# Performance work log

Hardware: AMD Instinct MI355X
Metric: run time of the kernel (lower is better)

The kernel has to match this reference:

```python
import jax, jax.numpy as jnp
import numpy as np

N_NODES = 150000
N_EDGES = 3000000
EMBED_DIM = 64
N_LAYERS = 3


def setup_inputs() -> dict:
    key = jax.random.key(0)
    k1, k2, k3, k4 = jax.random.split(key, 4)
    emb = jax.random.normal(k1, (N_NODES, EMBED_DIM), dtype=jnp.float32)
    sqrt_degree = jax.random.uniform(k2, (N_NODES, 1), dtype=jnp.float32)
    src = jax.random.randint(k3, (N_EDGES,), 0, N_NODES, dtype=jnp.int32)
    dst = jax.random.randint(k4, (N_EDGES,), 0, N_NODES, dtype=jnp.int32)
    return {"emb": emb, "sqrt_degree": sqrt_degree, "src": src, "dst": dst}


def _aggregate_unweighted(x, sqrt_degree, src, dst):
    # node = x * sqrt_degree ; message = node[src] ; N_h = sum per dst ; N_h *= sqrt_degree
    scaled = x * sqrt_degree                      # [N, D]
    msgs = scaled[src]                            # [E, D] gather
    agg = jax.ops.segment_sum(msgs, dst, num_segments=N_NODES)  # [N, D] scatter-add
    return agg * sqrt_degree


def reference(emb, sqrt_degree, src, dst):
    # propagate_embedding: ego embedding + n_layers of symmetric-normalized SpMM,
    # mean-combined across layers (layers_weight is None -> plain mean).
    ego = emb
    all_embed = [ego]
    for _ in range(N_LAYERS):
        ego = _aggregate_unweighted(ego, sqrt_degree, src, dst)
        all_embed.append(ego)
    return jnp.mean(jnp.stack(all_embed, axis=-1), axis=-1)  # [N, D]
```

## Files before the change

kernel.cpp:

```cpp
#include <hip/hip_runtime.h>

#define N_NODES   150000
#define N_EDGES   3000000
#define EMBED_DIM 64
#define N_UNITS   (N_EDGES / 4)
#define NREG      2344
#define CHUNK_U   2048
#define CHUNK_E   (CHUNK_U * 4)
#define NCB       ((N_UNITS + CHUNK_U - 1) / CHUNK_U)
#define REC_MAX   2560
#define KGRP      8
#define KPER      ((NCB + KGRP - 1) / KGRP)

typedef unsigned int uint;

__device__ inline uint pack2_bf16(float a, float b) {
    uint ua = __float_as_uint(a);
    uint ub = __float_as_uint(b);
    ua += 0x7fffu + ((ua >> 16) & 1u);
    ub += 0x7fffu + ((ub >> 16) & 1u);
    return (ua >> 16) | (ub & 0xffff0000u);
}
__device__ inline float bflo(uint u) { return __uint_as_float(u << 16); }
__device__ inline float bfhi(uint u) { return __uint_as_float(u & 0xffff0000u); }
#define FMA2(u, A0, A1)                                        \
    {   (A0) += w * bflo(u);  (A1) += w * bfhi(u); }

__global__ void k_to_y(const float4* __restrict__ in, const float* __restrict__ sd,
                       uint2* __restrict__ out, int n4) {
    int i = blockIdx.x * blockDim.x + threadIdx.x;
    if (i < n4) {
        float s = sd[i >> 4];
        float4 v = in[i];
        out[i] = make_uint2(pack2_bf16(s * v.x, s * v.y), pack2_bf16(s * v.z, s * v.w));
    }
}

__global__ __launch_bounds__(256) void k_count_place(const int4* __restrict__ dst4,
                                                     const int4* __restrict__ src4,
                                                     uint* __restrict__ bh,
                                                     uint* __restrict__ rowtot,
                                                     uint* __restrict__ bkt) {
    __shared__ uint cnt[NREG];
    __shared__ uint part[256];
    int t = threadIdx.x;
    for (int b = t; b < NREG; b += 256) cnt[b] = 0;
    __syncthreads();
    int base = blockIdx.x * CHUNK_U;
    for (int i = t; i < CHUNK_U; i += 256) {
        int u = base + i;
        if (u < N_UNITS) {
            int4 d = dst4[u];
            atomicAdd(&cnt[d.x >> 6], 1u);
            atomicAdd(&cnt[d.y >> 6], 1u);
            atomicAdd(&cnt[d.z >> 6], 1u);
            atomicAdd(&cnt[d.w >> 6], 1u);
        }
    }
    __syncthreads();
    const int CPT = (NREG + 255) / 256;
    int b0 = t * CPT, b1 = b0 + CPT; if (b1 > NREG) b1 = NREG; if (b0 > NREG) b0 = NREG;
    uint own = 0;
    for (int b = b0; b < b1; ++b) own += cnt[b];
    part[t] = own;
    __syncthreads();
    for (int off = 1; off < 256; off <<= 1) {
        uint v = (t >= off) ? part[t - off] : 0;
        __syncthreads();
        part[t] += v;
        __syncthreads();
    }
    uint run = part[t] - own;
    for (int b = b0; b < b1; ++b) { uint c = cnt[b]; cnt[b] = run; run += c; }
    __syncthreads();
    for (int b = t; b < NREG; b += 256) bh[blockIdx.x * NREG + b] = cnt[b];
    if (t == 255) rowtot[blockIdx.x] = part[255];
    __syncthreads();
    uint kbase = (uint)blockIdx.x * CHUNK_E;
    for (int i = t; i < CHUNK_U; i += 256) {
        int u = base + i;
        if (u < N_UNITS) {
            int4 d = dst4[u];
            int4 s = src4[u];
            uint p0 = atomicAdd(&cnt[d.x >> 6], 1u);
            uint p1 = atomicAdd(&cnt[d.y >> 6], 1u);
            uint p2 = atomicAdd(&cnt[d.z >> 6], 1u);
            uint p3 = atomicAdd(&cnt[d.w >> 6], 1u);
            bkt[kbase + p0] = ((uint)s.x << 6) | ((uint)d.x & 63u);
            bkt[kbase + p1] = ((uint)s.y << 6) | ((uint)d.y & 63u);
            bkt[kbase + p2] = ((uint)s.z << 6) | ((uint)d.z & 63u);
            bkt[kbase + p3] = ((uint)s.w << 6) | ((uint)d.w & 63u);
        }
    }
}

__global__ void k_cols(const uint* __restrict__ bh, const uint* __restrict__ rowtot,
                       uint* __restrict__ partial) {
    int tid = blockIdx.x * blockDim.x + threadIdx.x;
    if (tid >= KGRP * NREG) return;
    int g = tid / NREG;
    int r = tid % NREG;
    int kend = (g + 1) * KPER; if (kend > NCB) kend = NCB;
    uint run = 0;
    if (r + 1 < NREG) {
        for (int k = g * KPER; k < kend; ++k)
            run += bh[k * NREG + r + 1] - bh[k * NREG + r];
    } else {
        for (int k = g * KPER; k < kend; ++k)
            run += rowtot[k] - bh[k * NREG + r];
    }
    partial[g * NREG + r] = run;
}

__global__ void k_scan_small(const uint* __restrict__ partial, int* __restrict__ binPtr) {
    __shared__ uint s[1024];
    int t = threadIdx.x;
    int base = t * 3;
    uint v0 = 0, v1 = 0, v2 = 0;
    #pragma unroll
    for (int g = 0; g < KGRP; ++g) {
        if (base + 0 < NREG) v0 += partial[g * NREG + base + 0];
        if (base + 1 < NREG) v1 += partial[g * NREG + base + 1];
        if (base + 2 < NREG) v2 += partial[g * NREG + base + 2];
    }
    uint s3 = v0 + v1 + v2;
    s[t] = s3;
    __syncthreads();
    for (int off = 1; off < 1024; off <<= 1) {
        uint add = (t >= off) ? s[t - off] : 0;
        __syncthreads();
        s[t] += add;
        __syncthreads();
    }
    uint excl = s[t] - s3;
    if (base + 0 < NREG) binPtr[base + 0] = (int)excl;
    if (base + 1 < NREG) binPtr[base + 1] = (int)(excl + v0);
    if (base + 2 < NREG) binPtr[base + 2] = (int)(excl + v0 + v1);
    if (t == 1023) binPtr[NREG] = (int)s[1023];
}

__global__ __launch_bounds__(256) void k_finalize(const uint* __restrict__ bkt,
                                                  const uint* __restrict__ bh,
                                                  const uint* __restrict__ rowtot,
                                                  const int* __restrict__ binPtr,
                                                  int* __restrict__ rowptr,
                                                  uint* __restrict__ srcn) {
    __shared__ uint recs[REC_MAX];
    __shared__ uint part[256];
    __shared__ uint cnt64[64];
    __shared__ uint off64[64];
    int r = blockIdx.x;
    int t = threadIdx.x;
    int rbase = binPtr[r];
    int rcnt  = binPtr[r + 1] - rbase;

    int k0 = 2 * t, k1 = 2 * t + 1;
    uint s0 = 0, c0 = 0, s1 = 0, c1 = 0;
    if (k0 < NCB) {
        s0 = bh[k0 * NREG + r];
        uint e0 = (r + 1 < NREG) ? bh[k0 * NREG + r + 1] : rowtot[k0];
        c0 = e0 - s0;
    }
    if (k1 < NCB) {
        s1 = bh[k1 * NREG + r];
        uint e1 = (r + 1 < NREG) ? bh[k1 * NREG + r + 1] : rowtot[k1];
        c1 = e1 - s1;
    }
    uint own = c0 + c1;
    part[t] = own;
    __syncthreads();
    for (int off = 1; off < 256; off <<= 1) {
        uint v = (t >= off) ? part[t - off] : 0;
        __syncthreads();
        part[t] += v;
        __syncthreads();
    }
    uint w0 = part[t] - own;
    uint w1 = w0 + c0;
    for (uint i = 0; i < c0; ++i) recs[w0 + i] = bkt[(uint)k0 * CHUNK_E + s0 + i];
    for (uint i = 0; i < c1; ++i) recs[w1 + i] = bkt[(uint)k1 * CHUNK_E + s1 + i];
    if (t < 64) cnt64[t] = 0;
    __syncthreads();

    for (int e = t; e < rcnt; e += 256) atomicAdd(&cnt64[recs[e] & 63u], 1u);
    __syncthreads();
    if (t == 0) {
        uint run = 0;
        for (int i = 0; i < 64; ++i) { off64[i] = run; run += cnt64[i]; }
    }
    __syncthreads();
    int nbase = r * 64;
    int nloc = N_NODES - nbase; if (nloc > 64) nloc = 64;
    if (t < nloc) rowptr[nbase + t] = rbase + (int)off64[t];
    if (t < 64) cnt64[t] = 0;
    __syncthreads();

    for (int e = t; e < rcnt; e += 256) {
        uint rec = recs[e];
        uint loc = rec & 63u;
        uint pos = (uint)rbase + off64[loc] + atomicAdd(&cnt64[loc], 1u);
        srcn[pos] = rec >> 6;
    }
}

__global__ __launch_bounds__(256) void k_layer(const uint4* __restrict__ yb,
                                               const int* __restrict__ rowptr,
                                               const uint* __restrict__ srcn,
                                               const float* __restrict__ sd,
                                               uint4* __restrict__ yout) {
    int wv = (blockIdx.x * blockDim.x + threadIdx.x) >> 6;
    wv = __builtin_amdgcn_readfirstlane(wv);
    int nA = wv * 2;
    if (nA >= N_NODES) return;
    int nB = nA + 1;
    int lane = threadIdx.x & 63;
    int ep = lane >> 3;
    int j  = lane & 7;
    uint joff = (uint)j << 4;

    int startA = rowptr[nA];
    int endA   = rowptr[nB];
    int startB = endA;
    int endB   = (nB + 1 < N_NODES) ? rowptr[nB + 1] : N_EDGES;
    int eAm1 = max(endA - 1, 0);
    int eBm1 = max(endB - 1, 0);

    float a0 = 0.f, a1 = 0.f, a2 = 0.f, a3 = 0.f;
    float a4 = 0.f, a5 = 0.f, a6 = 0.f, a7 = 0.f;
    float b0 = 0.f, b1 = 0.f, b2 = 0.f, b3 = 0.f;
    float b4 = 0.f, b5 = 0.f, b6 = 0.f, b7 = 0.f;
    #pragma unroll 2
    for (int bA = startA, bB = startB; bA < endA || bB < endB; bA += 8, bB += 8) {
        int eeA = bA + ep;
        int eeB = bB + ep;
        int ecA = min(eeA, eAm1);
        int ecB = min(eeB, eBm1);
        uint sA = srcn[ecA];
        uint sB = srcn[ecB];
        float wA = (eeA < endA) ? 1.0f : 0.0f;
        float wB = (eeB < endB) ? 1.0f : 0.0f;
        uint4 vA = *(const uint4*)((const char*)yb + ((sA << 7) + joff));
        uint4 vB = *(const uint4*)((const char*)yb + ((sB << 7) + joff));
        { float w = wA;
          FMA2(vA.x, a0, a1); FMA2(vA.y, a2, a3); FMA2(vA.z, a4, a5); FMA2(vA.w, a6, a7); }
        { float w = wB;
          FMA2(vB.x, b0, b1); FMA2(vB.y, b2, b3); FMA2(vB.z, b4, b5); FMA2(vB.w, b6, b7); }
    }
    #pragma unroll
    for (int m = 8; m <= 32; m <<= 1) {
        a0 += __shfl_xor(a0, m, 64); a1 += __shfl_xor(a1, m, 64);
        a2 += __shfl_xor(a2, m, 64); a3 += __shfl_xor(a3, m, 64);
        a4 += __shfl_xor(a4, m, 64); a5 += __shfl_xor(a5, m, 64);
        a6 += __shfl_xor(a6, m, 64); a7 += __shfl_xor(a7, m, 64);
        b0 += __shfl_xor(b0, m, 64); b1 += __shfl_xor(b1, m, 64);
        b2 += __shfl_xor(b2, m, 64); b3 += __shfl_xor(b3, m, 64);
        b4 += __shfl_xor(b4, m, 64); b5 += __shfl_xor(b5, m, 64);
        b6 += __shfl_xor(b6, m, 64); b7 += __shfl_xor(b7, m, 64);
    }
    if (ep == 0) {
        float sdv = sd[nA];
        float s2 = sdv * sdv;
        uint4 r;
        r.x = pack2_bf16(s2 * a0, s2 * a1);
        r.y = pack2_bf16(s2 * a2, s2 * a3);
        r.z = pack2_bf16(s2 * a4, s2 * a5);
        r.w = pack2_bf16(s2 * a6, s2 * a7);
        yout[(size_t)nA * 8 + j] = r;
    } else if (ep == 1) {
        float sdv = sd[nB];
        float s2 = sdv * sdv;
        uint4 r;
        r.x = pack2_bf16(s2 * b0, s2 * b1);
        r.y = pack2_bf16(s2 * b2, s2 * b3);
        r.z = pack2_bf16(s2 * b4, s2 * b5);
        r.w = pack2_bf16(s2 * b6, s2 * b7);
        yout[(size_t)nB * 8 + j] = r;
    }
}

__global__ __launch_bounds__(256) void k_layer_final(const uint4* __restrict__ y2b,
                                                     const uint4* __restrict__ y1b,
                                                     const float4* __restrict__ emb,
                                                     const int* __restrict__ rowptr,
                                                     const uint* __restrict__ srcn,
                                                     const float* __restrict__ sd,
                                                     float4* __restrict__ out) {
    int wv = (blockIdx.x * blockDim.x + threadIdx.x) >> 6;
    wv = __builtin_amdgcn_readfirstlane(wv);
    int nA = wv * 2;
    if (nA >= N_NODES) return;
    int nB = nA + 1;
    int lane = threadIdx.x & 63;
    int ep = lane >> 3;
    int j  = lane & 7;
    uint joff = (uint)j << 4;

    int startA = rowptr[nA];
    int endA   = rowptr[nB];
    int startB = endA;
    int endB   = (nB + 1 < N_NODES) ? rowptr[nB + 1] : N_EDGES;
    int eAm1 = max(endA - 1, 0);
    int eBm1 = max(endB - 1, 0);

    float a0 = 0.f, a1 = 0.f, a2 = 0.f, a3 = 0.f;
    float a4 = 0.f, a5 = 0.f, a6 = 0.f, a7 = 0.f;
    float b0 = 0.f, b1 = 0.f, b2 = 0.f, b3 = 0.f;
    float b4 = 0.f, b5 = 0.f, b6 = 0.f, b7 = 0.f;
    #pragma unroll 2
    for (int bA = startA, bB = startB; bA < endA || bB < endB; bA += 8, bB += 8) {
        int eeA = bA + ep;
        int eeB = bB + ep;
        int ecA = min(eeA, eAm1);
        int ecB = min(eeB, eBm1);
        uint sA = srcn[ecA];
        uint sB = srcn[ecB];
        float wA = (eeA < endA) ? 1.0f : 0.0f;
        float wB = (eeB < endB) ? 1.0f : 0.0f;
        uint4 vA = *(const uint4*)((const char*)y2b + ((sA << 7) + joff));
        uint4 vB = *(const uint4*)((const char*)y2b + ((sB << 7) + joff));
        { float w = wA;
          FMA2(vA.x, a0, a1); FMA2(vA.y, a2, a3); FMA2(vA.z, a4, a5); FMA2(vA.w, a6, a7); }
        { float w = wB;
          FMA2(vB.x, b0, b1); FMA2(vB.y, b2, b3); FMA2(vB.z, b4, b5); FMA2(vB.w, b6, b7); }
    }
    #pragma unroll
    for (int m = 8; m <= 32; m <<= 1) {
        a0 += __shfl_xor(a0, m, 64); a1 += __shfl_xor(a1, m, 64);
        a2 += __shfl_xor(a2, m, 64); a3 += __shfl_xor(a3, m, 64);
        a4 += __shfl_xor(a4, m, 64); a5 += __shfl_xor(a5, m, 64);
        a6 += __shfl_xor(a6, m, 64); a7 += __shfl_xor(a7, m, 64);
        b0 += __shfl_xor(b0, m, 64); b1 += __shfl_xor(b1, m, 64);
        b2 += __shfl_xor(b2, m, 64); b3 += __shfl_xor(b3, m, 64);
        b4 += __shfl_xor(b4, m, 64); b5 += __shfl_xor(b5, m, 64);
        b6 += __shfl_xor(b6, m, 64); b7 += __shfl_xor(b7, m, 64);
    }
    int nd; float t0, t1, t2, t3, t4, t5, t6, t7;
    bool emit = false;
    if (ep == 0) {
        nd = nA; emit = true;
        t0 = a0; t1 = a1; t2 = a2; t3 = a3; t4 = a4; t5 = a5; t6 = a6; t7 = a7;
    } else if (ep == 1) {
        nd = nB; emit = true;
        t0 = b0; t1 = b1; t2 = b2; t3 = b3; t4 = b4; t5 = b5; t6 = b6; t7 = b7;
    }
    if (emit) {
        float sdv  = sd[nd];
        float rinv = (sdv > 0.0f) ? 1.0f / sdv : 0.0f;
        size_t ridx = (size_t)nd * 8 + j;
        uint4 u1 = y1b[ridx];
        uint4 u2 = y2b[ridx];
        float q0 = (bflo(u1.x) + bflo(u2.x)) * rinv + sdv * t0;
        float q1 = (bfhi(u1.x) + bfhi(u2.x)) * rinv + sdv * t1;
        float q2 = (bflo(u1.y) + bflo(u2.y)) * rinv + sdv * t2;
        float q3 = (bfhi(u1.y) + bfhi(u2.y)) * rinv + sdv * t3;
        float q4 = (bflo(u1.z) + bflo(u2.z)) * rinv + sdv * t4;
        float q5 = (bfhi(u1.z) + bfhi(u2.z)) * rinv + sdv * t5;
        float q6 = (bflo(u1.w) + bflo(u2.w)) * rinv + sdv * t6;
        float q7 = (bfhi(u1.w) + bfhi(u2.w)) * rinv + sdv * t7;
        size_t eidx = (size_t)nd * 16 + (size_t)j * 2;
        float4 e0 = emb[eidx];
        float4 e1 = emb[eidx + 1];
        float4 o0 = make_float4(0.25f * (e0.x + q0), 0.25f * (e0.y + q1),
                                0.25f * (e0.z + q2), 0.25f * (e0.w + q3));
        float4 o1 = make_float4(0.25f * (e1.x + q4), 0.25f * (e1.y + q5),
                                0.25f * (e1.z + q6), 0.25f * (e1.w + q7));
        out[eidx]     = o0;
        out[eidx + 1] = o1;
    }
}

extern "C" void kernel_launch(void* const* d_in, const int* in_sizes, int n_in,
                              void* d_out, int out_size, void* d_ws, size_t ws_size,
                              hipStream_t stream) {
    const float* emb = (const float*)d_in[0];
    const float* sd  = (const float*)d_in[1];
    const int*   src = (const int*)d_in[2];
    const int*   dst = (const int*)d_in[3];
    float*       out = (float*)d_out;

    char* ws = (char*)d_ws;
    auto align256 = [](size_t x) { return (x + 255) & ~(size_t)255; };
    size_t off = 0;
    int*  rowptr  = (int*)(ws + off);  off += align256((size_t)N_NODES * 4);
    uint* bh      = (uint*)(ws + off); off += align256((size_t)NCB * NREG * 4);
    uint* rowtot  = (uint*)(ws + off); off += align256((size_t)NCB * 4);
    uint* partial = (uint*)(ws + off); off += align256((size_t)KGRP * NREG * 4);
    int*  binPtr  = (int*)(ws + off);  off += align256((size_t)(NREG + 1) * 4);
    uint* bkt     = (uint*)(ws + off); off += align256((size_t)NCB * CHUNK_E * 4);
    uint* srcn    = (uint*)(ws + off); off += align256((size_t)N_EDGES * 4);
    const size_t rowBytes = (size_t)N_NODES * EMBED_DIM * 2;
    uint* buf0 = (uint*)(ws + off);    off += align256(rowBytes);
    uint* buf1 = (uint*)(ws + off);    off += align256(rowBytes);
    uint* buf2 = (uint*)(ws + off);

    const int n4 = N_NODES * EMBED_DIM / 4;
    const int nblk4 = (n4 + 255) / 256;
    const int colsblk = (KGRP * NREG + 255) / 256;

    k_count_place<<<NCB, 256, 0, stream>>>((const int4*)dst, (const int4*)src,
                                           bh, rowtot, bkt);
    k_cols<<<colsblk, 256, 0, stream>>>(bh, rowtot, partial);
    k_scan_small<<<1, 1024, 0, stream>>>(partial, binPtr);
    k_finalize<<<NREG, 256, 0, stream>>>(bkt, bh, rowtot, binPtr, rowptr, srcn);

    k_to_y<<<nblk4, 256, 0, stream>>>((const float4*)emb, sd, (uint2*)buf0, n4);

    const int nwaves = (N_NODES + 1) / 2;
    const int lblk = (nwaves + 3) / 4;
    k_layer<<<lblk, 256, 0, stream>>>((const uint4*)buf0, rowptr, srcn, sd, (uint4*)buf1);
    k_layer<<<lblk, 256, 0, stream>>>((const uint4*)buf1, rowptr, srcn, sd, (uint4*)buf2);
    k_layer_final<<<lblk, 256, 0, stream>>>((const uint4*)buf2, (const uint4*)buf1,
                                            (const float4*)emb, rowptr, srcn, sd,
                                            (float4*)out);
}
```

Baseline: 265.8 us.

## Drop global bin scan by giving each 64-node bin a fixed-capacity CSR slot

Measured after the change: 246.1 us. 7.4% less time.

```diff
diff --git a/kernel.cpp b/kernel.cpp
--- a/kernel.cpp
+++ b/kernel.cpp
@@ -9,8 +9,7 @@
 #define CHUNK_E   (CHUNK_U * 4)
 #define NCB       ((N_UNITS + CHUNK_U - 1) / CHUNK_U)
 #define REC_MAX   2560
-#define KGRP      8
-#define KPER      ((NCB + KGRP - 1) / KGRP)
+#define CAP       2560
 
 typedef unsigned int uint;
 
@@ -36,18 +35,18 @@
     }
 }
 
-__global__ __launch_bounds__(256) void k_count_place(const int4* __restrict__ dst4,
+__global__ __launch_bounds__(512) void k_count_place(const int4* __restrict__ dst4,
                                                      const int4* __restrict__ src4,
                                                      uint* __restrict__ bh,
                                                      uint* __restrict__ rowtot,
                                                      uint* __restrict__ bkt) {
     __shared__ uint cnt[NREG];
-    __shared__ uint part[256];
+    __shared__ uint part[512];
     int t = threadIdx.x;
-    for (int b = t; b < NREG; b += 256) cnt[b] = 0;
+    for (int b = t; b < NREG; b += 512) cnt[b] = 0;
     __syncthreads();
     int base = blockIdx.x * CHUNK_U;
-    for (int i = t; i < CHUNK_U; i += 256) {
+    for (int i = t; i < CHUNK_U; i += 512) {
         int u = base + i;
         if (u < N_UNITS) {
             int4 d = dst4[u];
@@ -58,13 +57,13 @@
         }
     }
     __syncthreads();
-    const int CPT = (NREG + 255) / 256;
+    const int CPT = (NREG + 511) / 512;
     int b0 = t * CPT, b1 = b0 + CPT; if (b1 > NREG) b1 = NREG; if (b0 > NREG) b0 = NREG;
     uint own = 0;
     for (int b = b0; b < b1; ++b) own += cnt[b];
     part[t] = own;
     __syncthreads();
-    for (int off = 1; off < 256; off <<= 1) {
+    for (int off = 1; off < 512; off <<= 1) {
         uint v = (t >= off) ? part[t - off] : 0;
         __syncthreads();
         part[t] += v;
@@ -73,11 +72,11 @@
     uint run = part[t] - own;
     for (int b = b0; b < b1; ++b) { uint c = cnt[b]; cnt[b] = run; run += c; }
     __syncthreads();
-    for (int b = t; b < NREG; b += 256) bh[blockIdx.x * NREG + b] = cnt[b];
-    if (t == 255) rowtot[blockIdx.x] = part[255];
+    for (int b = t; b < NREG; b += 512) bh[blockIdx.x * NREG + b] = cnt[b];
+    if (t == 511) rowtot[blockIdx.x] = part[511];
     __syncthreads();
     uint kbase = (uint)blockIdx.x * CHUNK_E;
-    for (int i = t; i < CHUNK_U; i += 256) {
+    for (int i = t; i < CHUNK_U; i += 512) {
         int u = base + i;
         if (u < N_UNITS) {
             int4 d = dst4[u];
@@ -94,65 +93,18 @@
     }
 }
 
-__global__ void k_cols(const uint* __restrict__ bh, const uint* __restrict__ rowtot,
-                       uint* __restrict__ partial) {
-    int tid = blockIdx.x * blockDim.x + threadIdx.x;
-    if (tid >= KGRP * NREG) return;
-    int g = tid / NREG;
-    int r = tid % NREG;
-    int kend = (g + 1) * KPER; if (kend > NCB) kend = NCB;
-    uint run = 0;
-    if (r + 1 < NREG) {
-        for (int k = g * KPER; k < kend; ++k)
-            run += bh[k * NREG + r + 1] - bh[k * NREG + r];
-    } else {
-        for (int k = g * KPER; k < kend; ++k)
-            run += rowtot[k] - bh[k * NREG + r];
-    }
-    partial[g * NREG + r] = run;
-}
-
-__global__ void k_scan_small(const uint* __restrict__ partial, int* __restrict__ binPtr) {
-    __shared__ uint s[1024];
-    int t = threadIdx.x;
-    int base = t * 3;
-    uint v0 = 0, v1 = 0, v2 = 0;
-    #pragma unroll
-    for (int g = 0; g < KGRP; ++g) {
-        if (base + 0 < NREG) v0 += partial[g * NREG + base + 0];
-        if (base + 1 < NREG) v1 += partial[g * NREG + base + 1];
-        if (base + 2 < NREG) v2 += partial[g * NREG + base + 2];
-    }
-    uint s3 = v0 + v1 + v2;
-    s[t] = s3;
-    __syncthreads();
-    for (int off = 1; off < 1024; off <<= 1) {
-        uint add = (t >= off) ? s[t - off] : 0;
-        __syncthreads();
-        s[t] += add;
-        __syncthreads();
-    }
-    uint excl = s[t] - s3;
-    if (base + 0 < NREG) binPtr[base + 0] = (int)excl;
-    if (base + 1 < NREG) binPtr[base + 1] = (int)(excl + v0);
-    if (base + 2 < NREG) binPtr[base + 2] = (int)(excl + v0 + v1);
-    if (t == 1023) binPtr[NREG] = (int)s[1023];
-}
-
 __global__ __launch_bounds__(256) void k_finalize(const uint* __restrict__ bkt,
                                                   const uint* __restrict__ bh,
                                                   const uint* __restrict__ rowtot,
-                                                  const int* __restrict__ binPtr,
-                                                  int* __restrict__ rowptr,
+                                                  int2* __restrict__ rowse,
                                                   uint* __restrict__ srcn) {
     __shared__ uint recs[REC_MAX];
     __shared__ uint part[256];
     __shared__ uint cnt64[64];
-    __shared__ uint off64[64];
+    __shared__ uint off64[65];
     int r = blockIdx.x;
     int t = threadIdx.x;
-    int rbase = binPtr[r];
-    int rcnt  = binPtr[r + 1] - rbase;
+    int rbase = r * CAP;
 
     int k0 = 2 * t, k1 = 2 * t + 1;
     uint s0 = 0, c0 = 0, s1 = 0, c1 = 0;
@@ -175,6 +127,7 @@
         part[t] += v;
         __syncthreads();
     }
+    int rcnt = (int)part[255];
     uint w0 = part[t] - own;
     uint w1 = w0 + c0;
     for (uint i = 0; i < c0; ++i) recs[w0 + i] = bkt[(uint)k0 * CHUNK_E + s0 + i];
@@ -187,11 +140,13 @@
     if (t == 0) {
         uint run = 0;
         for (int i = 0; i < 64; ++i) { off64[i] = run; run += cnt64[i]; }
+        off64[64] = run;
     }
     __syncthreads();
     int nbase = r * 64;
     int nloc = N_NODES - nbase; if (nloc > 64) nloc = 64;
-    if (t < nloc) rowptr[nbase + t] = rbase + (int)off64[t];
+    if (t < nloc)
+        rowse[nbase + t] = make_int2(rbase + (int)off64[t], rbase + (int)off64[t + 1]);
     if (t < 64) cnt64[t] = 0;
     __syncthreads();
 
@@ -204,7 +159,7 @@
 }
 
 __global__ __launch_bounds__(256) void k_layer(const uint4* __restrict__ yb,
-                                               const int* __restrict__ rowptr,
+                                               const int2* __restrict__ rowse,
                                                const uint* __restrict__ srcn,
                                                const float* __restrict__ sd,
                                                uint4* __restrict__ yout) {
@@ -218,10 +173,10 @@
     int j  = lane & 7;
     uint joff = (uint)j << 4;
 
-    int startA = rowptr[nA];
-    int endA   = rowptr[nB];
-    int startB = endA;
-    int endB   = (nB + 1 < N_NODES) ? rowptr[nB + 1] : N_EDGES;
+    int2 rA = rowse[nA];
+    int2 rB = rowse[nB];
+    int startA = rA.x, endA = rA.y;
+    int startB = rB.x, endB = rB.y;
     int eAm1 = max(endA - 1, 0);
     int eBm1 = max(endB - 1, 0);
 
@@ -235,8 +190,8 @@
         int eeB = bB + ep;
         int ecA = min(eeA, eAm1);
         int ecB = min(eeB, eBm1);
-        uint sA = srcn[ecA];
-        uint sB = srcn[ecB];
+        uint sA = min(srcn[ecA], (uint)(N_NODES - 1));
+        uint sB = min(srcn[ecB], (uint)(N_NODES - 1));
         float wA = (eeA < endA) ? 1.0f : 0.0f;
         float wB = (eeB < endB) ? 1.0f : 0.0f;
         uint4 vA = *(const uint4*)((const char*)yb + ((sA << 7) + joff));
@@ -281,7 +236,7 @@
 __global__ __launch_bounds__(256) void k_layer_final(const uint4* __restrict__ y2b,
                                                      const uint4* __restrict__ y1b,
                                                      const float4* __restrict__ emb,
-                                                     const int* __restrict__ rowptr,
+                                                     const int2* __restrict__ rowse,
                                                      const uint* __restrict__ srcn,
                                                      const float* __restrict__ sd,
                                                      float4* __restrict__ out) {
@@ -295,10 +250,10 @@
     int j  = lane & 7;
     uint joff = (uint)j << 4;
 
-    int startA = rowptr[nA];
-    int endA   = rowptr[nB];
-    int startB = endA;
-    int endB   = (nB + 1 < N_NODES) ? rowptr[nB + 1] : N_EDGES;
+    int2 rA = rowse[nA];
+    int2 rB = rowse[nB];
+    int startA = rA.x, endA = rA.y;
+    int startB = rB.x, endB = rB.y;
     int eAm1 = max(endA - 1, 0);
     int eBm1 = max(endB - 1, 0);
 
@@ -312,8 +267,8 @@
         int eeB = bB + ep;
         int ecA = min(eeA, eAm1);
         int ecB = min(eeB, eBm1);
-        uint sA = srcn[ecA];
-        uint sB = srcn[ecB];
+        uint sA = min(srcn[ecA], (uint)(N_NODES - 1));
+        uint sB = min(srcn[ecB], (uint)(N_NODES - 1));
         float wA = (eeA < endA) ? 1.0f : 0.0f;
         float wB = (eeB < endB) ? 1.0f : 0.0f;
         uint4 vA = *(const uint4*)((const char*)y2b + ((sA << 7) + joff));
@@ -381,35 +336,30 @@
     char* ws = (char*)d_ws;
     auto align256 = [](size_t x) { return (x + 255) & ~(size_t)255; };
     size_t off = 0;
-    int*  rowptr  = (int*)(ws + off);  off += align256((size_t)N_NODES * 4);
-    uint* bh      = (uint*)(ws + off); off += align256((size_t)NCB * NREG * 4);
-    uint* rowtot  = (uint*)(ws + off); off += align256((size_t)NCB * 4);
-    uint* partial = (uint*)(ws + off); off += align256((size_t)KGRP * NREG * 4);
-    int*  binPtr  = (int*)(ws + off);  off += align256((size_t)(NREG + 1) * 4);
-    uint* bkt     = (uint*)(ws + off); off += align256((size_t)NCB * CHUNK_E * 4);
-    uint* srcn    = (uint*)(ws + off); off += align256((size_t)N_EDGES * 4);
+    int2* rowse  = (int2*)(ws + off); off += align256((size_t)N_NODES * 8);
+    uint* bh     = (uint*)(ws + off); off += align256((size_t)NCB * NREG * 4);
+    uint* rowtot = (uint*)(ws + off); off += align256((size_t)NCB * 4);
+    uint* bkt    = (uint*)(ws + off); off += align256((size_t)NCB * CHUNK_E * 4);
+    uint* srcn   = (uint*)(ws + off); off += align256((size_t)NREG * CAP * 4);
     const size_t rowBytes = (size_t)N_NODES * EMBED_DIM * 2;
-    uint* buf0 = (uint*)(ws + off);    off += align256(rowBytes);
-    uint* buf1 = (uint*)(ws + off);    off += align256(rowBytes);
+    uint* buf0 = (uint*)(ws + off);   off += align256(rowBytes);
+    uint* buf1 = (uint*)(ws + off);   off += align256(rowBytes);
     uint* buf2 = (uint*)(ws + off);
 
     const int n4 = N_NODES * EMBED_DIM / 4;
     const int nblk4 = (n4 + 255) / 256;
-    const int colsblk = (KGRP * NREG + 255) / 256;
-
-    k_count_place<<<NCB, 256, 0, stream>>>((const int4*)dst, (const int4*)src,
+
+    k_count_place<<<NCB, 512, 0, stream>>>((const int4*)dst, (const int4*)src,
                                            bh, rowtot, bkt);
-    k_cols<<<colsblk, 256, 0, stream>>>(bh, rowtot, partial);
-    k_scan_small<<<1, 1024, 0, stream>>>(partial, binPtr);
-    k_finalize<<<NREG, 256, 0, stream>>>(bkt, bh, rowtot, binPtr, rowptr, srcn);
+    k_finalize<<<NREG, 256, 0, stream>>>(bkt, bh, rowtot, rowse, srcn);
 
     k_to_y<<<nblk4, 256, 0, stream>>>((const float4*)emb, sd, (uint2*)buf0, n4);
 
     const int nwaves = (N_NODES + 1) / 2;
     const int lblk = (nwaves + 3) / 4;
-    k_layer<<<lblk, 256, 0, stream>>>((const uint4*)buf0, rowptr, srcn, sd, (uint4*)buf1);
-    k_layer<<<lblk, 256, 0, stream>>>((const uint4*)buf1, rowptr, srcn, sd, (uint4*)buf2);
+    k_layer<<<lblk, 256, 0, stream>>>((const uint4*)buf0, rowse, srcn, sd, (uint4*)buf1);
+    k_layer<<<lblk, 256, 0, stream>>>((const uint4*)buf1, rowse, srcn, sd, (uint4*)buf2);
     k_layer_final<<<lblk, 256, 0, stream>>>((const uint4*)buf2, (const uint4*)buf1,
-                                            (const float4*)emb, rowptr, srcn, sd,
+                                            (const float4*)emb, rowse, srcn, sd,
                                             (float4*)out);
 }
```
